# Kernel optimization log

Hardware: AMD Instinct MI355X
Metric: run time of the kernel (lower is better)

The kernel has to match this reference:

```python
import jax, jax.numpy as jnp
import numpy as np

N = 50000   # nodes
E = 800000  # edges
IN, H1, H2, OUT = 256, 512, 1024, 3000
EPS = 1e-5


def _glorot(key, fan_in, fan_out):
    s = jnp.sqrt(6.0 / (fan_in + fan_out)).astype(jnp.float32)
    return jax.random.uniform(key, (fan_in, fan_out), jnp.float32, -s, s)


def setup_inputs() -> dict:
    key = jax.random.key(0)
    ks = jax.random.split(key, 8)
    x = jax.random.normal(ks[0], (N, IN), jnp.float32)
    edge_index = jax.random.randint(ks[1], (2, E), 0, N, jnp.int64)
    edge_attr = jax.random.uniform(ks[2], (E, 3), jnp.float32)
    y = jnp.zeros((N,), jnp.int64)  # single domain -> plain BatchNorm path
    return {
        "x": x, "edge_index": edge_index, "edge_attr": edge_attr, "y": y,
        "W1": _glorot(ks[3], IN, H1), "b1": jnp.zeros((H1,), jnp.float32),
        "g1": jnp.ones((H1,), jnp.float32), "be1": jnp.zeros((H1,), jnp.float32),
        "W2": _glorot(ks[4], H1, H2), "b2": jnp.zeros((H2,), jnp.float32),
        "g2": jnp.ones((H2,), jnp.float32), "be2": jnp.zeros((H2,), jnp.float32),
        "W3": _glorot(ks[5], H2, OUT), "b3": jnp.zeros((OUT,), jnp.float32),
    }


def _gcn_layer(h_in, W, b, src, dst, w):
    # PyG GCNConv: x' = D^{-1/2}(A_w + I)D^{-1/2} x W + b, self-loop weight 1
    h = h_in @ W                                             # [N, F]
    deg = jax.ops.segment_sum(w, dst, num_segments=N) + 1.0  # weighted in-degree + self loop
    dinv = jax.lax.rsqrt(deg)                                # [N]
    coef = dinv[src] * w * dinv[dst]                         # [E]
    agg = jax.ops.segment_sum(coef[:, None] * h[src], dst, num_segments=N)
    return agg + (dinv * dinv)[:, None] * h + b              # self-loop term + bias


def _bn_relu(h, g, b):
    # BatchNorm1d in training mode (batch statistics, biased variance) + ReLU
    m = h.mean(axis=0)
    v = jnp.mean((h - m) ** 2, axis=0)
    return jax.nn.relu((h - m) * jax.lax.rsqrt(v + EPS) * g + b)


def reference(x, edge_index, edge_attr, y, W1, b1, g1, be1, W2, b2, g2, be2, W3, b3):
    src, dst = edge_index[0], edge_index[1]
    w = edge_attr[:, 2]
    h = _bn_relu(_gcn_layer(x, W1, b1, src, dst, w), g1, be1)
    h = _bn_relu(_gcn_layer(h, W2, b2, src, dst, w), g2, be2)
    return _gcn_layer(h, W3, b3, src, dst, w)
```

## Files before the change

### kernel.cpp

```cpp
#include <hip/hip_runtime.h>

#define NN 50000
#define NE 800000
#define EPSV 1e-5f

typedef _Float16 f16;
typedef __attribute__((ext_vector_type(4)))  float f32x4;
typedef __attribute__((ext_vector_type(16))) float f32x16;
typedef __attribute__((ext_vector_type(8)))  f16 f16x8;
typedef __attribute__((ext_vector_type(4)))  f16 f16x4;

static __device__ __forceinline__ int kperm(int k){
  int q = (k>>2)&3;
  int p = ((q&1)<<1) | (q>>1);
  return (k & ~15) + (p<<2) + (k&3);
}

__global__ void k_init_deg(float* __restrict__ deg){
  int i = blockIdx.x*256 + threadIdx.x;
  if (i < NN) deg[i] = 1.0f;
}

__global__ void k_build(const int* __restrict__ ei, const float* __restrict__ ea,
                        int* __restrict__ cnt, float* __restrict__ deg){
  int e = blockIdx.x*256 + threadIdx.x;
  if (e < NE){
    int d = ei[NE + e];
    atomicAdd(&cnt[d], 1);
    atomicAdd(&deg[d], ea[3*e+2]);
  }
}

__global__ void k_fin_deg(const float* __restrict__ deg, float* __restrict__ dinv,
                          float* __restrict__ dinv2){
  int i = blockIdx.x*256 + threadIdx.x;
  if (i < NN){ float r = rsqrtf(deg[i]); dinv[i] = r; dinv2[i] = r*r; }
}

__global__ __launch_bounds__(1024) void k_scan(const int* __restrict__ cnt,
                                               int* __restrict__ rowptr,
                                               int* __restrict__ cursor){
  __shared__ int sums[1024];
  int t = threadIdx.x;
  int b0 = t*49, b1 = b0+49; if (b0 > NN) b0 = NN; if (b1 > NN) b1 = NN;
  int s = 0;
  for (int i = b0; i < b1; ++i) s += cnt[i];
  sums[t] = s; __syncthreads();
  for (int o = 1; o < 1024; o <<= 1){
    int v = (t >= o) ? sums[t-o] : 0;
    __syncthreads();
    sums[t] += v;
    __syncthreads();
  }
  int p = sums[t] - s;
  for (int i = b0; i < b1; ++i){ rowptr[i] = p; cursor[i] = p; p += cnt[i]; }
  if (t == 1023) rowptr[NN] = sums[1023];
}

__global__ void k_fill(const int* __restrict__ ei, const float* __restrict__ ea,
                       const float* __restrict__ dinv, int* __restrict__ cursor,
                       int* __restrict__ csrc, float* __restrict__ ccf){
  int e = blockIdx.x*256 + threadIdx.x;
  if (e < NE){
    int s = ei[e], d = ei[NE+e];
    float w = ea[3*e+2];
    int p = atomicAdd(&cursor[d], 1);
    csrc[p] = s;
    ccf[p] = dinv[s]*w*dinv[d];
  }
}

__global__ void k_xconv(const float* __restrict__ x, f16* __restrict__ xh){
  int idx = blockIdx.x*256 + threadIdx.x;
  if (idx >= NN*64) return;
  int node = idx >> 6, k = (idx & 63)*4;
  f32x4 v = *(const f32x4*)(x + (size_t)node*256 + k);
  f16x4 h;
  #pragma unroll
  for (int j=0;j<4;++j) h[j] = (f16)v[j];
  *(f16x4*)(xh + (size_t)node*256 + kperm(k)) = h;
}

__global__ void k_w16(const float* __restrict__ W, f16* __restrict__ Wt,
                      int K, int M, int Mpad){
  int idx = blockIdx.x*256 + threadIdx.x;
  if (idx >= K*Mpad) return;
  int k = idx / Mpad, n = idx % Mpad;
  float v = (n < M) ? W[(size_t)k*M + n] : 0.f;
  Wt[(size_t)n*K + kperm(k)] = (f16)v;
}

template<int K, bool BN>
__global__ __launch_bounds__(256) void k_agg16(
    const f16* __restrict__ H, const int* __restrict__ rp,
    const int* __restrict__ cs, const float* __restrict__ cf,
    const float* __restrict__ dinv2,
    const float* __restrict__ s1, const float* __restrict__ s2,
    const float* __restrict__ g, const float* __restrict__ be,
    f16* __restrict__ outp)
{
  const int tid = threadIdx.x;
  int node, c;
  if (K == 256){
    node = blockIdx.x*8 + (tid>>5);
    c = (tid&31)*8;
  } else {
    node = blockIdx.x*4 + (tid>>6);
    c = (blockIdx.y<<9) + (tid&63)*8;
  }
  if (node >= NN) return;
  float av[8], bv[8];
  if (BN){
    int qa0 = kperm(c), qa1 = kperm(c+4);
    #pragma unroll
    for (int j=0;j<8;++j){
      int ac = (j<4) ? qa0+j : qa1+(j-4);
      float mm = s1[c+j]*(1.f/NN);
      float var = s2[c+j]*(1.f/NN) - mm*mm;
      float sc = rsqrtf(var+EPSV)*g[ac];
      av[j] = sc;
      bv[j] = fmaf(-mm, sc, be[ac]);
    }
  }
  f16x8 hv = *(const f16x8*)(H + (size_t)node*K + c);
  float d2 = dinv2[node];
  float acc[8];
  #pragma unroll
  for (int j=0;j<8;++j){
    float v = (float)hv[j];
    if (BN){ v = fmaf(v, av[j], bv[j]); v = v > 0.f ? v : 0.f; }
    acc[j] = d2*v;
  }
  int e0 = rp[node], e1 = rp[node+1];
  for (int e = e0; e < e1; ++e){
    int s = cs[e]; float w = cf[e];
    f16x8 v8 = *(const f16x8*)(H + (size_t)s*K + c);
    #pragma unroll
    for (int j=0;j<8;++j){
      float v = (float)v8[j];
      if (BN){ v = fmaf(v, av[j], bv[j]); v = v > 0.f ? v : 0.f; }
      acc[j] += w*v;
    }
  }
  f16x8 o;
  #pragma unroll
  for (int j=0;j<8;++j) o[j] = (f16)acc[j];
  *(f16x8*)(outp + (size_t)node*K + c) = o;
}

template<bool STATS>
__global__ __launch_bounds__(512,2) void k_gemm512(
    const f16* __restrict__ A, const f16* __restrict__ B,
    const float* __restrict__ bias, float* __restrict__ Cf,
    f16* __restrict__ Ch, float* __restrict__ s1, float* __restrict__ s2,
    int K, int M)
{
  __shared__ f16 Ah[2][8192];
  __shared__ f16 Bh[2][8192];
  const int tid  = threadIdx.x;
  const int lane = tid & 63;
  const int wave = tid >> 6;
  const int wr = wave >> 2;
  const int wc = wave & 3;

  const int gx = gridDim.x, gy = gridDim.y;
  int bid = blockIdx.y*gx + blockIdx.x;
  int nwg8 = (gx*gy) >> 3;
  int L = (bid & 7)*nwg8 + (bid >> 3);
  const int by = L / gx, bx = L % gx;
  const int row0 = by*256, col0 = bx*256;

  f32x16 acc[4][2];
  #pragma unroll
  for (int m=0;m<4;++m)
    #pragma unroll
    for (int n=0;n<2;++n)
      #pragma unroll
      for (int t=0;t<16;++t) acc[m][n][t] = 0.f;

  auto stage = [&](int buf, int k0){
    #pragma unroll
    for (int i=0;i<2;++i){
      int phys = i*512 + tid;
      int rr = phys >> 2, cp = phys & 3;
      int sc2 = cp ^ ((rr>>1)&3);
      const f16* srcA = A + (size_t)(row0+rr)*K + k0 + sc2*8;
      const f16* srcB = B + (size_t)(col0+rr)*K + k0 + sc2*8;
      f16* dstA = &Ah[buf][(size_t)(i*512 + (wave<<6))*8];
      f16* dstB = &Bh[buf][(size_t)(i*512 + (wave<<6))*8];
      __builtin_amdgcn_global_load_lds((const unsigned int*)srcA, (unsigned int*)dstA, 16, 0, 0);
      __builtin_amdgcn_global_load_lds((const unsigned int*)srcB, (unsigned int*)dstB, 16, 0, 0);
    }
  };

  stage(0, 0);
  __syncthreads();
  const int nT = K >> 5;
  for (int t = 0; t < nT; ++t){
    const int cur = t & 1;
    if (t + 1 < nT) stage(cur^1, (t+1) << 5);

    const int hg = lane >> 5;
    const int rl = lane & 31;
    #pragma unroll
    for (int c2=0;c2<2;++c2){
      const int u = c2*2 + hg;
      f16x8 fa[4], fb[2];
      #pragma unroll
      for (int m=0;m<4;++m){
        int r = wr*128 + m*32 + rl;
        fa[m] = *(const f16x8*)&Ah[cur][r*32 + ((u ^ ((r>>1)&3))<<3)];
      }
      #pragma unroll
      for (int n=0;n<2;++n){
        int r = wc*64 + n*32 + rl;
        fb[n] = *(const f16x8*)&Bh[cur][r*32 + ((u ^ ((r>>1)&3))<<3)];
      }
      #pragma unroll
      for (int m=0;m<4;++m)
        #pragma unroll
        for (int n=0;n<2;++n)
          acc[m][n] = __builtin_amdgcn_mfma_f32_32x32x16_f16(fa[m], fb[n], acc[m][n], 0,0,0);
    }
    __syncthreads();
  }

  #pragma unroll
  for (int n=0;n<2;++n){
    int cg = col0 + wc*64 + n*32 + (lane&31);
    if (STATS){
      int cp = kperm(cg);
      float sum = 0.f, sq = 0.f;
      #pragma unroll
      for (int m=0;m<4;++m){
        #pragma unroll
        for (int t=0;t<16;++t){
          int rg = row0 + wr*128 + m*32 + (t&3) + ((t>>2)&3)*8 + ((lane>>5)<<2);
          if (rg < NN){
            float v = acc[m][n][t];
            sum += v; sq += v*v;
            Ch[(size_t)rg*M + cp] = (f16)v;
          }
        }
      }
      atomicAdd(&s1[cp], sum);
      atomicAdd(&s2[cp], sq);
    } else {
      float bv = (cg < M) ? bias[cg] : 0.f;
      #pragma unroll
      for (int m=0;m<4;++m){
        #pragma unroll
        for (int t=0;t<16;++t){
          int rg = row0 + wr*128 + m*32 + (t&3) + ((t>>2)&3)*8 + ((lane>>5)<<2);
          if (rg < NN && cg < M)
            __builtin_nontemporal_store(acc[m][n][t] + bv, &Cf[(size_t)rg*M + cg]);
        }
      }
    }
  }
}

extern "C" void kernel_launch(void* const* d_in, const int* in_sizes, int n_in,
                              void* d_out, int out_size, void* d_ws, size_t ws_size,
                              hipStream_t stream){
  const float* x   = (const float*)d_in[0];
  const int*   ei  = (const int*)d_in[1];
  const float* ea  = (const float*)d_in[2];
  const float* W1  = (const float*)d_in[4];
  const float* g1  = (const float*)d_in[6];
  const float* be1 = (const float*)d_in[7];
  const float* W2  = (const float*)d_in[8];
  const float* g2  = (const float*)d_in[10];
  const float* be2 = (const float*)d_in[11];
  const float* W3  = (const float*)d_in[12];
  const float* b3  = (const float*)d_in[13];
  float* out = (float*)d_out;

  char* p = (char*)d_ws;
  int*   cnt    = (int*)p;   p += (size_t)NN*4;
  int*   cursor = (int*)p;   p += (size_t)NN*4;
  int*   rowptr = (int*)p;   p += (size_t)(NN+4)*4;
  float* deg    = (float*)p; p += (size_t)NN*4;
  float* dinv   = (float*)p; p += (size_t)NN*4;
  float* dinv2  = (float*)p; p += (size_t)NN*4;
  int*   csrc   = (int*)p;   p += (size_t)NE*4;
  float* ccf    = (float*)p; p += (size_t)NE*4;
  f16*   Wt     = (f16*)p;   p += (size_t)3072*1024*2;
  float* s1a    = (float*)p; p += 1024*4;
  float* s2a    = (float*)p; p += 1024*4;
  float* s1b    = (float*)p; p += 1024*4;
  float* s2b    = (float*)p; p += 1024*4;
  f16*   aggh   = (f16*)p;   p += (size_t)50176*1024*2;

  f16* xh  = (f16*)out;
  f16* h1h = xh  + (size_t)NN*256;
  f16* h2h = h1h + (size_t)NN*512;

  const int T = 256;
  const int gN = (NN+T-1)/T, gE = NE/T;
  const int GR = 196;

  hipMemsetAsync(cnt, 0, (size_t)NN*4, stream);
  hipMemsetAsync(s1a, 0, 4*1024*4, stream);
  k_init_deg<<<gN,T,0,stream>>>(deg);
  k_build<<<gE,T,0,stream>>>(ei, ea, cnt, deg);
  k_fin_deg<<<gN,T,0,stream>>>(deg, dinv, dinv2);
  k_scan<<<1,1024,0,stream>>>(cnt, rowptr, cursor);
  k_fill<<<gE,T,0,stream>>>(ei, ea, dinv, cursor, csrc, ccf);
  k_xconv<<<(NN*64+T-1)/T,T,0,stream>>>(x, xh);

  k_agg16<256,false><<<dim3(NN/8,1),T,0,stream>>>(xh, rowptr, csrc, ccf, dinv2,
                                                  nullptr,nullptr,nullptr,nullptr, aggh);
  k_w16<<<(256*512)/T,T,0,stream>>>(W1, Wt, 256, 512, 512);
  k_gemm512<true><<<dim3(2,GR),512,0,stream>>>(aggh, Wt, nullptr, nullptr, h1h, s1a, s2a, 256, 512);

  k_agg16<512,true><<<dim3(NN/4,1),T,0,stream>>>(h1h, rowptr, csrc, ccf, dinv2,
                                                 s1a, s2a, g1, be1, aggh);
  k_w16<<<(512*1024)/T,T,0,stream>>>(W2, Wt, 512, 1024, 1024);
  k_gemm512<true><<<dim3(4,GR),512,0,stream>>>(aggh, Wt, nullptr, nullptr, h2h, s1b, s2b, 512, 1024);

  k_agg16<1024,true><<<dim3(NN/4,2),T,0,stream>>>(h2h, rowptr, csrc, ccf, dinv2,
                                                  s1b, s2b, g2, be2, aggh);
  k_w16<<<(1024*3072)/T,T,0,stream>>>(W3, Wt, 1024, 3000, 3072);
  k_gemm512<false><<<dim3(12,GR),512,0,stream>>>(aggh, Wt, b3, out, nullptr, nullptr, nullptr, 1024, 3000);
}
```

Measured before the change: 1.560 ms.

## Retile GEMM to 256x128 blocks with triple-buffered async LDS pipeline

The MFMA GEMM moves from 512-thread 256x256 tiles with a double buffer to 256-thread 256x128 tiles with a three-slot LDS ring. Each step waits with explicit vmcnt counts, so up to two future K-slices stay in flight while the current one is computed. This replaces the full syncthreads drain with raw barriers. The aim is to hide global-to-LDS latency and raise block count and occupancy. In exchange, the B tile is reused less per A load, so there is more global traffic per FLOP.

```diff
diff --git a/kernel.cpp b/kernel.cpp
--- a/kernel.cpp
+++ b/kernel.cpp
@@ -149,26 +149,26 @@
 }
 
 template<bool STATS>
-__global__ __launch_bounds__(512,2) void k_gemm512(
+__global__ __launch_bounds__(256,2) void k_gemmr(
     const f16* __restrict__ A, const f16* __restrict__ B,
     const float* __restrict__ bias, float* __restrict__ Cf,
     f16* __restrict__ Ch, float* __restrict__ s1, float* __restrict__ s2,
     int K, int M)
 {
-  __shared__ f16 Ah[2][8192];
-  __shared__ f16 Bh[2][8192];
+  __shared__ f16 Ah[3][8192];
+  __shared__ f16 Bh[3][4096];
   const int tid  = threadIdx.x;
   const int lane = tid & 63;
   const int wave = tid >> 6;
-  const int wr = wave >> 2;
-  const int wc = wave & 3;
+  const int wr = wave >> 1;
+  const int wc = wave & 1;
 
   const int gx = gridDim.x, gy = gridDim.y;
   int bid = blockIdx.y*gx + blockIdx.x;
   int nwg8 = (gx*gy) >> 3;
   int L = (bid & 7)*nwg8 + (bid >> 3);
   const int by = L / gx, bx = L % gx;
-  const int row0 = by*256, col0 = bx*256;
+  const int row0 = by*256, col0 = bx*128;
 
   f32x16 acc[4][2];
   #pragma unroll
@@ -178,30 +178,44 @@
       #pragma unroll
       for (int t=0;t<16;++t) acc[m][n][t] = 0.f;
 
-  auto stage = [&](int buf, int k0){
-    #pragma unroll
-    for (int i=0;i<2;++i){
-      int phys = i*512 + tid;
+  auto stage = [&](int slot, int k0){
+    #pragma unroll
+    for (int i=0;i<4;++i){
+      int phys = i*256 + tid;
       int rr = phys >> 2, cp = phys & 3;
       int sc2 = cp ^ ((rr>>1)&3);
       const f16* srcA = A + (size_t)(row0+rr)*K + k0 + sc2*8;
+      f16* dstA = &Ah[slot][(size_t)(i*256 + (wave<<6))*8];
+      __builtin_amdgcn_global_load_lds((const unsigned int*)srcA, (unsigned int*)dstA, 16, 0, 0);
+    }
+    #pragma unroll
+    for (int i=0;i<2;++i){
+      int phys = i*256 + tid;
+      int rr = phys >> 2, cp = phys & 3;
+      int sc2 = cp ^ ((rr>>1)&3);
       const f16* srcB = B + (size_t)(col0+rr)*K + k0 + sc2*8;
-      f16* dstA = &Ah[buf][(size_t)(i*512 + (wave<<6))*8];
-      f16* dstB = &Bh[buf][(size_t)(i*512 + (wave<<6))*8];
-      __builtin_amdgcn_global_load_lds((const unsigned int*)srcA, (unsigned int*)dstA, 16, 0, 0);
+      f16* dstB = &Bh[slot][(size_t)(i*256 + (wave<<6))*8];
       __builtin_amdgcn_global_load_lds((const unsigned int*)srcB, (unsigned int*)dstB, 16, 0, 0);
     }
   };
 
+  const int nT = K >> 5;
   stage(0, 0);
-  __syncthreads();
-  const int nT = K >> 5;
+  stage(1, 32);
+  stage(2, 64);
+
+  int cur = 0;
   for (int t = 0; t < nT; ++t){
-    const int cur = t & 1;
-    if (t + 1 < nT) stage(cur^1, (t+1) << 5);
+    if (t + 2 < nT)      asm volatile("s_waitcnt vmcnt(12)" ::: "memory");
+    else if (t + 1 < nT) asm volatile("s_waitcnt vmcnt(6)" ::: "memory");
+    else                 asm volatile("s_waitcnt vmcnt(0)" ::: "memory");
+    __builtin_amdgcn_s_barrier();
+    __builtin_amdgcn_sched_barrier(0);
 
     const int hg = lane >> 5;
     const int rl = lane & 31;
+    const f16* Ab = &Ah[cur][0];
+    const f16* Bb = &Bh[cur][0];
     #pragma unroll
     for (int c2=0;c2<2;++c2){
       const int u = c2*2 + hg;
@@ -209,12 +223,12 @@
       #pragma unroll
       for (int m=0;m<4;++m){
         int r = wr*128 + m*32 + rl;
-        fa[m] = *(const f16x8*)&Ah[cur][r*32 + ((u ^ ((r>>1)&3))<<3)];
+        fa[m] = *(const f16x8*)&Ab[r*32 + ((u ^ ((r>>1)&3))<<3)];
       }
       #pragma unroll
       for (int n=0;n<2;++n){
         int r = wc*64 + n*32 + rl;
-        fb[n] = *(const f16x8*)&Bh[cur][r*32 + ((u ^ ((r>>1)&3))<<3)];
+        fb[n] = *(const f16x8*)&Bb[r*32 + ((u ^ ((r>>1)&3))<<3)];
       }
       #pragma unroll
       for (int m=0;m<4;++m)
@@ -222,7 +236,10 @@
         for (int n=0;n<2;++n)
           acc[m][n] = __builtin_amdgcn_mfma_f32_32x32x16_f16(fa[m], fb[n], acc[m][n], 0,0,0);
     }
-    __syncthreads();
+    __builtin_amdgcn_s_barrier();
+    __builtin_amdgcn_sched_barrier(0);
+    if (t + 3 < nT) stage(cur, (t+3) << 5);
+    cur = (cur == 2) ? 0 : cur + 1;
   }
 
   #pragma unroll
@@ -312,15 +329,15 @@
   k_agg16<256,false><<<dim3(NN/8,1),T,0,stream>>>(xh, rowptr, csrc, ccf, dinv2,
                                                   nullptr,nullptr,nullptr,nullptr, aggh);
   k_w16<<<(256*512)/T,T,0,stream>>>(W1, Wt, 256, 512, 512);
-  k_gemm512<true><<<dim3(2,GR),512,0,stream>>>(aggh, Wt, nullptr, nullptr, h1h, s1a, s2a, 256, 512);
+  k_gemmr<true><<<dim3(4,GR),T,0,stream>>>(aggh, Wt, nullptr, nullptr, h1h, s1a, s2a, 256, 512);
 
   k_agg16<512,true><<<dim3(NN/4,1),T,0,stream>>>(h1h, rowptr, csrc, ccf, dinv2,
                                                  s1a, s2a, g1, be1, aggh);
   k_w16<<<(512*1024)/T,T,0,stream>>>(W2, Wt, 512, 1024, 1024);
-  k_gemm512<true><<<dim3(4,GR),512,0,stream>>>(aggh, Wt, nullptr, nullptr, h2h, s1b, s2b, 512, 1024);
+  k_gemmr<true><<<dim3(8,GR),T,0,stream>>>(aggh, Wt, nullptr, nullptr, h2h, s1b, s2b, 512, 1024);
 
   k_agg16<1024,true><<<dim3(NN/4,2),T,0,stream>>>(h2h, rowptr, csrc, ccf, dinv2,
                                                   s1b, s2b, g2, be2, aggh);
   k_w16<<<(1024*3072)/T,T,0,stream>>>(W3, Wt, 1024, 3000, 3072);
-  k_gemm512<false><<<dim3(12,GR),512,0,stream>>>(aggh, Wt, b3, out, nullptr, nullptr, nullptr, 1024, 3000);
-}
+  k_gemmr<false><<<dim3(24,GR),T,0,stream>>>(aggh, Wt, b3, out, nullptr, nullptr, nullptr, 1024, 3000);
+}
```

Result: slower. 1.606 ms (+2.9%).

## Deepen GEMM LDS pipeline to four stages with explicit vmcnt waits

Applied to the files above, without the earlier changes.

The GEMM moves from double-buffered LDS staging to a 4-slot ring with prefetch three tiles ahead. It uses explicit s_waitcnt vmcnt counts and a single raw barrier per iteration instead of a full __syncthreads, and splits the A and B prefetches across the two k-substeps. MFMA blocks are wrapped in s_setprio. The aim is to hide global-load latency better, at the cost of doubling LDS use to 128KB and cutting occupancy to one block per CU, with tighter correctness reliance on the vmcnt counts.

```diff
diff --git a/kernel.cpp b/kernel.cpp
--- a/kernel.cpp
+++ b/kernel.cpp
@@ -149,14 +149,14 @@
 }
 
 template<bool STATS>
-__global__ __launch_bounds__(512,2) void k_gemm512(
+__global__ __launch_bounds__(512,1) void k_gemm512(
     const f16* __restrict__ A, const f16* __restrict__ B,
     const float* __restrict__ bias, float* __restrict__ Cf,
     f16* __restrict__ Ch, float* __restrict__ s1, float* __restrict__ s2,
     int K, int M)
 {
-  __shared__ f16 Ah[2][8192];
-  __shared__ f16 Bh[2][8192];
+  __shared__ f16 Ah[4][8192];
+  __shared__ f16 Bh[4][8192];
   const int tid  = threadIdx.x;
   const int lane = tid & 63;
   const int wave = tid >> 6;
@@ -178,51 +178,74 @@
       #pragma unroll
       for (int t=0;t<16;++t) acc[m][n][t] = 0.f;
 
-  auto stage = [&](int buf, int k0){
+  auto stageA = [&](int slot, int k0){
     #pragma unroll
     for (int i=0;i<2;++i){
       int phys = i*512 + tid;
       int rr = phys >> 2, cp = phys & 3;
       int sc2 = cp ^ ((rr>>1)&3);
       const f16* srcA = A + (size_t)(row0+rr)*K + k0 + sc2*8;
+      f16* dstA = &Ah[slot][(size_t)(i*512 + (wave<<6))*8];
+      __builtin_amdgcn_global_load_lds((const unsigned int*)srcA, (unsigned int*)dstA, 16, 0, 0);
+    }
+  };
+  auto stageB = [&](int slot, int k0){
+    #pragma unroll
+    for (int i=0;i<2;++i){
+      int phys = i*512 + tid;
+      int rr = phys >> 2, cp = phys & 3;
+      int sc2 = cp ^ ((rr>>1)&3);
       const f16* srcB = B + (size_t)(col0+rr)*K + k0 + sc2*8;
-      f16* dstA = &Ah[buf][(size_t)(i*512 + (wave<<6))*8];
-      f16* dstB = &Bh[buf][(size_t)(i*512 + (wave<<6))*8];
-      __builtin_amdgcn_global_load_lds((const unsigned int*)srcA, (unsigned int*)dstA, 16, 0, 0);
+      f16* dstB = &Bh[slot][(size_t)(i*512 + (wave<<6))*8];
       __builtin_amdgcn_global_load_lds((const unsigned int*)srcB, (unsigned int*)dstB, 16, 0, 0);
     }
   };
 
-  stage(0, 0);
-  __syncthreads();
   const int nT = K >> 5;
+  stageA(0,0);  stageB(0,0);
+  stageA(1,32); stageB(1,32);
+  stageA(2,64); stageB(2,64);
+
+  const int hg = lane >> 5;
+  const int rl = lane & 31;
   for (int t = 0; t < nT; ++t){
-    const int cur = t & 1;
-    if (t + 1 < nT) stage(cur^1, (t+1) << 5);
-
-    const int hg = lane >> 5;
-    const int rl = lane & 31;
+    const int cur = t & 3;
+    if (t + 2 < nT)      asm volatile("s_waitcnt vmcnt(8)" ::: "memory");
+    else if (t + 1 < nT) asm volatile("s_waitcnt vmcnt(4)" ::: "memory");
+    else                 asm volatile("s_waitcnt vmcnt(0)" ::: "memory");
+    __builtin_amdgcn_sched_barrier(0);
+    __builtin_amdgcn_s_barrier();
+    __builtin_amdgcn_sched_barrier(0);
+
+    const bool pf = (t + 3 < nT);
+    const int  ps = (t + 3) & 3;
+    const int  pk = (t + 3) << 5;
+    const f16* Ab = &Ah[cur][0];
+    const f16* Bb = &Bh[cur][0];
     #pragma unroll
     for (int c2=0;c2<2;++c2){
+      if (c2 == 0){ if (pf) stageA(ps, pk); }
+      else        { if (pf) stageB(ps, pk); }
       const int u = c2*2 + hg;
       f16x8 fa[4], fb[2];
       #pragma unroll
       for (int m=0;m<4;++m){
         int r = wr*128 + m*32 + rl;
-        fa[m] = *(const f16x8*)&Ah[cur][r*32 + ((u ^ ((r>>1)&3))<<3)];
+        fa[m] = *(const f16x8*)&Ab[r*32 + ((u ^ ((r>>1)&3))<<3)];
       }
       #pragma unroll
       for (int n=0;n<2;++n){
         int r = wc*64 + n*32 + rl;
-        fb[n] = *(const f16x8*)&Bh[cur][r*32 + ((u ^ ((r>>1)&3))<<3)];
+        fb[n] = *(const f16x8*)&Bb[r*32 + ((u ^ ((r>>1)&3))<<3)];
       }
+      __builtin_amdgcn_s_setprio(1);
       #pragma unroll
       for (int m=0;m<4;++m)
         #pragma unroll
         for (int n=0;n<2;++n)
           acc[m][n] = __builtin_amdgcn_mfma_f32_32x32x16_f16(fa[m], fb[n], acc[m][n], 0,0,0);
-    }
-    __syncthreads();
+      __builtin_amdgcn_s_setprio(0);
+    }
   }
 
   #pragma unroll
```

New measurement: 1.621 ms. 1.04x slower.
